# Kernel tuning notes

Measured on AMD Instinct MI355X. Metric: run time of the kernel, lower is better.

The kernel has to match this reference:

```python
import jax, jax.numpy as jnp
import numpy as np

D_MODEL = 1024
D_STATE = 16
D_CONV = 4
EXPAND = 2
D_INNER = EXPAND * D_MODEL
DT_RANK = (D_MODEL + 15) // 16  # ceil(d_model/16) = 64
BATCH = 2
SEQLEN = 1024


def _causal_conv_silu(x, w, b):
    # x: (B, d_inner, L); w: (d_inner, 1, k) depthwise; causal left padding k-1
    k = w.shape[-1]
    y = jax.lax.conv_general_dilated(
        x, w, window_strides=(1,), padding=[(k - 1, 0)],
        dimension_numbers=("NCH", "OIH", "NCH"), feature_group_count=x.shape[1])
    return jax.nn.silu(y + b[None, :, None])


def _ssm_scan(dA, dBx):
    # h_t = dA_t * h_{t-1} + dBx_t, parallel associative scan over L (axis=2)
    def op(e1, e2):
        a1, b1 = e1
        a2, b2 = e2
        return (a1 * a2, a2 * b1 + b2)
    return jax.lax.associative_scan(op, (dA, dBx), axis=2)[1]


def _mamba_dir(xz, conv_w, conv_b, xproj_w, dtproj_w, dt_bias, A_log, Dp):
    d_inner = xz.shape[1] // 2
    x, z = xz[:, :d_inner], xz[:, d_inner:]
    u = _causal_conv_silu(x, conv_w, conv_b)                  # (B, d, L)
    x_dbl = jnp.einsum('bdl,kd->bkl', u, xproj_w)             # (B, dt_rank+2n, L)
    n = A_log.shape[1]
    r = dtproj_w.shape[1]
    delta = jnp.einsum('dr,brl->bdl', dtproj_w, x_dbl[:, :r])
    Bm = x_dbl[:, r:r + n]                                    # (B, n, L)
    Cm = x_dbl[:, r + n:]                                     # (B, n, L)
    delta = jax.nn.softplus(delta + dt_bias[None, :, None])
    A = -jnp.exp(A_log)                                       # (d, n)
    dA = jnp.exp(jnp.einsum('bdl,dn->bdln', delta, A))
    dBx = jnp.einsum('bdl,bnl,bdl->bdln', delta, Bm, u)
    h = _ssm_scan(dA, dBx)                                    # (B, d, L, n)
    y = jnp.einsum('bdln,bnl->bdl', h, Cm)
    y = y + Dp[None, :, None] * u
    return y * jax.nn.silu(z)


def setup_inputs() -> dict:
    key = jax.random.key(0)
    ks = jax.random.split(key, 16)
    s_in = 1.0 / np.sqrt(D_MODEL)
    s_x = 1.0 / np.sqrt(D_INNER)
    dt_std = DT_RANK ** -0.5

    def dt_bias_init(k):
        dt = jnp.exp(jax.random.uniform(k, (D_INNER,)) * (np.log(0.1) - np.log(0.001)) + np.log(0.001))
        dt = jnp.clip(dt, 1e-4, None)
        return dt + jnp.log(-jnp.expm1(-dt))  # inverse softplus

    A_log = jnp.log(jnp.tile(jnp.arange(1, D_STATE + 1, dtype=jnp.float32)[None, :], (D_INNER, 1)))
    inp = {
        'hidden_states': jax.random.normal(ks[0], (BATCH, SEQLEN, D_MODEL), jnp.float32),
        'in_proj_w': jax.random.normal(ks[1], (2 * D_INNER, D_MODEL), jnp.float32) * s_in,
        'conv_w': jax.random.normal(ks[2], (D_INNER, 1, D_CONV), jnp.float32) * 0.3,
        'conv_bias': jnp.zeros((D_INNER,), jnp.float32),
        'x_proj_w': jax.random.normal(ks[3], (DT_RANK + 2 * D_STATE, D_INNER), jnp.float32) * s_x,
        'dt_proj_w': jax.random.uniform(ks[4], (D_INNER, DT_RANK), jnp.float32, -dt_std, dt_std),
        'dt_proj_bias': dt_bias_init(ks[5]),
        'A_log': A_log,
        'D_skip': jnp.ones((D_INNER,), jnp.float32),
        'convb_w': jax.random.normal(ks[6], (D_INNER, 1, D_CONV), jnp.float32) * 0.3,
        'convb_bias': jnp.zeros((D_INNER,), jnp.float32),
        'x_proj_b_w': jax.random.normal(ks[7], (DT_RANK + 2 * D_STATE, D_INNER), jnp.float32) * s_x,
        'dt_proj_b_w': jax.random.uniform(ks[8], (D_INNER, DT_RANK), jnp.float32, -dt_std, dt_std),
        'dt_proj_b_bias': dt_bias_init(ks[9]),
        'A_b_log': A_log,
        'D_b_skip': jnp.ones((D_INNER,), jnp.float32),
        'out_proj_w': jax.random.normal(ks[10], (D_MODEL, D_INNER), jnp.float32) * s_x,
    }
    return inp


def reference(hidden_states, in_proj_w, conv_w, conv_bias, x_proj_w, dt_proj_w,
              dt_proj_bias, A_log, D_skip, convb_w, convb_bias, x_proj_b_w,
              dt_proj_b_w, dt_proj_b_bias, A_b_log, D_b_skip, out_proj_w):
    # in_proj (no bias): (B, 2*d_inner, L)
    xz = jnp.einsum('ed,bld->bel', in_proj_w, hidden_states)
    out_f = _mamba_dir(xz, conv_w, conv_bias, x_proj_w, dt_proj_w, dt_proj_bias, A_log, D_skip)
    out_b = _mamba_dir(xz[:, :, ::-1], convb_w, convb_bias, x_proj_b_w, dt_proj_b_w,
                       dt_proj_b_bias, A_b_log, D_b_skip)[:, :, ::-1]
    # if_divide_out=False: just sum then out_proj (no bias)
    return jnp.einsum('bdl,od->blo', out_f + out_b, out_proj_w)
```

## Files before the change

kernel.cpp:

```cpp
#include <hip/hip_runtime.h>
#include <math.h>


typedef _Float16 f16x8 __attribute__((ext_vector_type(8)));
typedef _Float16 f16x4 __attribute__((ext_vector_type(4)));
typedef float    f32x4 __attribute__((ext_vector_type(4)));

#define SCH 32
#define SCL 32

__device__ __forceinline__ void gload_lds16(const void* g, void* l) {
    __builtin_amdgcn_global_load_lds(
        (const __attribute__((address_space(1))) void*)g,
        (__attribute__((address_space(3))) void*)l, 16, 0, 0);
}

__device__ __forceinline__ float softplus_f(float x) {
    float e = __builtin_amdgcn_exp2f(-fabsf(x) * 1.44269504f);
    return fmaxf(x, 0.f) + __builtin_amdgcn_logf(1.f + e) * 0.69314718f;
}

template<int CTRL>
__device__ __forceinline__ float dpp_add(float x) {
    int s = __builtin_amdgcn_update_dpp(0, __builtin_bit_cast(int, x),
                                        CTRL, 0xF, 0xF, true);
    return x + __builtin_bit_cast(float, s);
}

template<int WMW, int WNW, int FM, int FN>
__global__ __launch_bounds__(256)
void gemm_nt_f16(const _Float16* __restrict__ A, const _Float16* __restrict__ B,
                 float* __restrict__ C, int K, int ldc, long sA, long sC)
{
    constexpr int BM = WMW * FM * 16, BN = WNW * FN * 16;
    constexpr int ACH = BM / 8, NCH = (BM + BN) / 8;
    __shared__ __align__(16) _Float16 lds[(BM + BN) * 64];
    A += (long)blockIdx.z * sA;
    C += (long)blockIdx.z * sC;
    const int m0 = blockIdx.y * BM, n0 = blockIdx.x * BN;
    const int t = threadIdx.x, wid = t >> 6, lane = t & 63;
    const int wm = wid / WNW, wn = wid % WNW;
    const int srow = lane >> 3;
    const int skk  = ((lane & 7) ^ srow) * 8;

    f32x4 acc[FM][FN];
#pragma unroll
    for (int i = 0; i < FM; ++i)
#pragma unroll
        for (int j = 0; j < FN; ++j) acc[i][j] = (f32x4){0.f, 0.f, 0.f, 0.f};

    for (int k0 = 0; k0 < K; k0 += 64) {
#pragma unroll
        for (int c = wid; c < NCH; c += 4) {
            const _Float16* gp = (c < ACH)
                ? A + (long)(m0 + c * 8 + srow) * K + k0 + skk
                : B + (long)(n0 + (c - ACH) * 8 + srow) * K + k0 + skk;
            gload_lds16(gp, lds + c * 512);
        }
        __syncthreads();
#pragma unroll
        for (int kw = 0; kw < 2; ++kw) {
            f16x8 af[FM], bf[FN];
#pragma unroll
            for (int i = 0; i < FM; ++i) {
                int r = wm * FM * 16 + i * 16 + (lane & 15);
                af[i] = *(const f16x8*)(lds + r * 64 +
                        (((kw * 4 + (lane >> 4)) ^ (r & 7)) * 8));
            }
#pragma unroll
            for (int j = 0; j < FN; ++j) {
                int r = wn * FN * 16 + j * 16 + (lane & 15);
                bf[j] = *(const f16x8*)(lds + BM * 64 + r * 64 +
                        (((kw * 4 + (lane >> 4)) ^ (r & 7)) * 8));
            }
#pragma unroll
            for (int i = 0; i < FM; ++i)
#pragma unroll
                for (int j = 0; j < FN; ++j)
                    acc[i][j] = __builtin_amdgcn_mfma_f32_16x16x32_f16(
                        af[i], bf[j], acc[i][j], 0, 0, 0);
        }
        __syncthreads();
    }
#pragma unroll
    for (int i = 0; i < FM; ++i)
#pragma unroll
        for (int j = 0; j < FN; ++j) {
            int n = n0 + wn * FN * 16 + j * 16 + (lane & 15);
            int m = m0 + wm * FM * 16 + i * 16 + (lane >> 4) * 4;
            *(f32x4*)&C[(long)n * ldc + m] = acc[i][j];
        }
}

#define XP_SK 8
__global__ __launch_bounds__(256)
void xproj_f16_kernel(const _Float16* __restrict__ u16, const _Float16* __restrict__ xw16,
                      float* __restrict__ pb)
{
    __shared__ __align__(16) _Float16 Asw[128 * 64];
    __shared__ __align__(16) _Float16 Bsw[96 * 64];
    const int t = threadIdx.x, wid = t >> 6, lane = t & 63;
    const int wm = wid >> 1, wn = wid & 1;
    const int m0 = blockIdx.x * 128;
    const int sk = blockIdx.y, dirb = blockIdx.z;
    const _Float16* ub = u16 + (long)dirb * 2048 * 1024;
    const _Float16* Bw = xw16 + (long)(dirb >> 1) * 96 * 2048;
    const int srow = lane >> 3;
    const int skk  = ((lane & 7) ^ srow) * 8;
    const int lloc = (t & 31) * 4;
    const int kslt = t >> 5;

    f32x4 acc[4][3];
#pragma unroll
    for (int i = 0; i < 4; ++i)
#pragma unroll
        for (int j = 0; j < 3; ++j) acc[i][j] = (f32x4){0.f, 0.f, 0.f, 0.f};

    for (int ks = 0; ks < 2048 / XP_SK; ks += 64) {
        const int k0 = sk * (2048 / XP_SK) + ks;
#pragma unroll
        for (int c = wid; c < 12; c += 4)
            gload_lds16(Bw + (long)(c * 8 + srow) * 2048 + k0 + skk, Bsw + c * 512);
        _Float16 av[8][4];
#pragma unroll
        for (int kk = 0; kk < 8; ++kk) {
            f16x4 v = *(const f16x4*)&ub[(long)(k0 + kslt * 8 + kk) * 1024 + m0 + lloc];
            av[kk][0] = v[0]; av[kk][1] = v[1]; av[kk][2] = v[2]; av[kk][3] = v[3];
        }
#pragma unroll
        for (int q = 0; q < 4; ++q) {
            int l = lloc + q;
            f16x8 h = {av[0][q], av[1][q], av[2][q], av[3][q],
                       av[4][q], av[5][q], av[6][q], av[7][q]};
            *(f16x8*)(Asw + l * 64 + ((kslt ^ (l & 7)) * 8)) = h;
        }
        __syncthreads();
#pragma unroll
        for (int kw = 0; kw < 2; ++kw) {
            f16x8 af[4], bf[3];
#pragma unroll
            for (int i = 0; i < 4; ++i) {
                int r = wm * 64 + i * 16 + (lane & 15);
                af[i] = *(const f16x8*)(Asw + r * 64 +
                        (((kw * 4 + (lane >> 4)) ^ (r & 7)) * 8));
            }
#pragma unroll
            for (int j = 0; j < 3; ++j) {
                int r = wn * 48 + j * 16 + (lane & 15);
                bf[j] = *(const f16x8*)(Bsw + r * 64 +
                        (((kw * 4 + (lane >> 4)) ^ (r & 7)) * 8));
            }
#pragma unroll
            for (int i = 0; i < 4; ++i)
#pragma unroll
                for (int j = 0; j < 3; ++j)
                    acc[i][j] = __builtin_amdgcn_mfma_f32_16x16x32_f16(
                        af[i], bf[j], acc[i][j], 0, 0, 0);
        }
        __syncthreads();
    }
    float* Cp = pb + ((long)sk * 4 + dirb) * 96 * 1024;
#pragma unroll
    for (int i = 0; i < 4; ++i)
#pragma unroll
        for (int j = 0; j < 3; ++j) {
            int n = wn * 48 + j * 16 + (lane & 15);
            int m = m0 + wm * 64 + i * 16 + (lane >> 4) * 4;
            *(f32x4*)&Cp[(long)n * 1024 + m] = acc[i][j];
        }
}

__global__ __launch_bounds__(256)
void xreduce_kernel(const float* __restrict__ pb, float* __restrict__ xdbl)
{
    int f = (blockIdx.x * 256 + threadIdx.x) * 4;
    f32x4 s = (f32x4){0.f, 0.f, 0.f, 0.f};
#pragma unroll
    for (int sk = 0; sk < XP_SK; ++sk)
        s += *(const f32x4*)(pb + (long)sk * 393216 + f);
    *(f32x4*)(xdbl + f) = s;
}

__global__ __launch_bounds__(256)
void dtproj_f16_kernel(const float* __restrict__ xdbl, const _Float16* __restrict__ dw16,
                       const float* __restrict__ bcat, _Float16* __restrict__ delta16)
{
    __shared__ __align__(16) _Float16 Asw[128 * 64];
    __shared__ __align__(16) _Float16 Bsw[128 * 64];
    const int t = threadIdx.x, wid = t >> 6, lane = t & 63;
    const int wm = wid >> 1, wn = wid & 1;
    const int n0 = blockIdx.x * 128, m0 = blockIdx.y * 128;
    const int dirb = blockIdx.z, dir = dirb >> 1;
    const float* Xb = xdbl + (long)dirb * 96 * 1024;
    const _Float16* Bw = dw16 + (long)dir * 2048 * 64;
    const int srow = lane >> 3, skk = ((lane & 7) ^ srow) * 8;
    const int lloc = (t & 31) * 4, kslt = t >> 5;

#pragma unroll
    for (int c = wid; c < 16; c += 4)
        gload_lds16(Bw + (long)(n0 + c * 8 + srow) * 64 + skk, Bsw + c * 512);
    float av[8][4];
#pragma unroll
    for (int kk = 0; kk < 8; ++kk) {
        f32x4 v = *(const f32x4*)&Xb[(long)(kslt * 8 + kk) * 1024 + m0 + lloc];
        av[kk][0] = v.x; av[kk][1] = v.y; av[kk][2] = v.z; av[kk][3] = v.w;
    }
#pragma unroll
    for (int q = 0; q < 4; ++q) {
        int l = lloc + q;
        f16x8 h = {(_Float16)av[0][q], (_Float16)av[1][q], (_Float16)av[2][q],
                   (_Float16)av[3][q], (_Float16)av[4][q], (_Float16)av[5][q],
                   (_Float16)av[6][q], (_Float16)av[7][q]};
        *(f16x8*)(Asw + l * 64 + ((kslt ^ (l & 7)) * 8)) = h;
    }
    __syncthreads();

    f32x4 acc[4][4];
#pragma unroll
    for (int i = 0; i < 4; ++i)
#pragma unroll
        for (int j = 0; j < 4; ++j) acc[i][j] = (f32x4){0.f, 0.f, 0.f, 0.f};
#pragma unroll
    for (int kw = 0; kw < 2; ++kw) {
        f16x8 af[4], bf[4];
#pragma unroll
        for (int i = 0; i < 4; ++i) {
            int r = wm * 64 + i * 16 + (lane & 15);
            af[i] = *(const f16x8*)(Asw + r * 64 +
                    (((kw * 4 + (lane >> 4)) ^ (r & 7)) * 8));
        }
#pragma unroll
        for (int j = 0; j < 4; ++j) {
            int r = wn * 64 + j * 16 + (lane & 15);
            bf[j] = *(const f16x8*)(Bsw + r * 64 +
                    (((kw * 4 + (lane >> 4)) ^ (r & 7)) * 8));
        }
#pragma unroll
        for (int i = 0; i < 4; ++i)
#pragma unroll
            for (int j = 0; j < 4; ++j)
                acc[i][j] = __builtin_amdgcn_mfma_f32_16x16x32_f16(
                    af[i], bf[j], acc[i][j], 0, 0, 0);
    }
    _Float16* Dp = delta16 + (long)dirb * 2048 * 1024;
#pragma unroll
    for (int j = 0; j < 4; ++j) {
        int dd = n0 + wn * 64 + j * 16 + (lane & 15);
        float bm = bcat[dir * 2048 + dd];
#pragma unroll
        for (int i = 0; i < 4; ++i) {
            int m = m0 + wm * 64 + i * 16 + (lane >> 4) * 4;
            f32x4 v = acc[i][j];
            f16x4 o = {(_Float16)softplus_f(v.x + bm), (_Float16)softplus_f(v.y + bm),
                       (_Float16)softplus_f(v.z + bm), (_Float16)softplus_f(v.w + bm)};
            *(f16x4*)&Dp[(long)dd * 1024 + m] = o;
        }
    }
}

__global__ __launch_bounds__(256)
void setup_kernel(const float* __restrict__ hidden, const float* __restrict__ winp,
                  const float* __restrict__ woutp,
                  const float* __restrict__ xwf, const float* __restrict__ xwb,
                  const float* __restrict__ dwf, const float* __restrict__ dwb,
                  const float* __restrict__ bf,  const float* __restrict__ bb,
                  _Float16* __restrict__ H16, _Float16* __restrict__ Win16,
                  _Float16* __restrict__ Wout16,
                  _Float16* __restrict__ xw16, _Float16* __restrict__ dw16,
                  float* __restrict__ bcat)
{
    long i4 = ((long)blockIdx.x * 256 + threadIdx.x) * 4;
    auto cvt4 = [](const float* s) -> f16x4 {
        float4 v = *(const float4*)s;
        return (f16x4){(_Float16)v.x, (_Float16)v.y, (_Float16)v.z, (_Float16)v.w};
    };
    if (i4 < 4194304) *(f16x4*)(Win16 + i4) = cvt4(winp + i4);
    if (i4 < 2097152) {
        *(f16x4*)(H16 + i4)   = cvt4(hidden + i4);
        *(f16x4*)(Wout16 + i4) = cvt4(woutp + i4);
    }
    if (i4 < 196608) {
        *(f16x4*)(xw16 + i4)          = cvt4(xwf + i4);
        *(f16x4*)(xw16 + 196608 + i4) = cvt4(xwb + i4);
    }
    if (i4 < 131072) {
        *(f16x4*)(dw16 + i4)          = cvt4(dwf + i4);
        *(f16x4*)(dw16 + 131072 + i4) = cvt4(dwb + i4);
    }
    if (i4 < 2048) {
        *(float4*)(bcat + i4)        = *(const float4*)(bf + i4);
        *(float4*)(bcat + 2048 + i4) = *(const float4*)(bb + i4);
    }
}

__global__ __launch_bounds__(256)
void conv_silu_kernel(const float* __restrict__ xz,
                      const float* __restrict__ wf, const float* __restrict__ bf,
                      const float* __restrict__ wb, const float* __restrict__ bbk,
                      _Float16* __restrict__ u16)
{
    long idx = (long)blockIdx.x * 256 + threadIdx.x;
    int l = (int)(idx & 1023);
    long r = idx >> 10;
    int d = (int)(r & 2047);
    int b = (int)((r >> 11) & 1);
    int dir = (int)(r >> 12);
    const float* x = xz + ((long)b * 4096 + d) * 1024;
    const float* w = dir ? wb : wf;
    float s = dir ? bbk[d] : bf[d];
    if (dir == 0) {
#pragma unroll
        for (int j = 0; j < 4; ++j) {
            int p = l - 3 + j;
            if (p >= 0) s = fmaf(w[d * 4 + j], x[p], s);
        }
    } else {
#pragma unroll
        for (int j = 0; j < 4; ++j) {
            int src = l - 3 + j;
            if (src >= 0) s = fmaf(w[d * 4 + j], x[1023 - src], s);
        }
    }
    u16[idx] = (_Float16)(s / (1.f + __builtin_amdgcn_exp2f(-s * 1.44269504f)));
}

__global__ __launch_bounds__(256)
void scan_p1_kernel(const _Float16* __restrict__ u16, const _Float16* __restrict__ delta16,
                    const float* __restrict__ xdbl,
                    const float* __restrict__ Alf, const float* __restrict__ Alb,
                    float* __restrict__ hend, float* __restrict__ aprod)
{
    __shared__ _Float16 sD[64][40], sU[64][40];
    __shared__ float sB[32][20];
    const int t = threadIdx.x, wid = t >> 6, lane = t & 63;
    const int nl = lane & 3;
    const int dloc = wid * 16 + (lane >> 2);
    const int dblk = blockIdx.x, chunk = blockIdx.y, dirb = blockIdx.z;
    const int d = dblk * 64 + dloc, dir = dirb >> 1;
    const int T0 = chunk * SCL;
    f32x4 Av = *(const f32x4*)((dir ? Alb : Alf) + d * 16 + nl * 4);
    float An2[4] = {-expf(Av.x) * 1.44269504f, -expf(Av.y) * 1.44269504f,
                    -expf(Av.z) * 1.44269504f, -expf(Av.w) * 1.44269504f};
    const _Float16* dp = delta16 + ((long)dirb * 2048 + dblk * 64) * 1024;
    const _Float16* up = u16    + ((long)dirb * 2048 + dblk * 64) * 1024;
    const float* Bp = xdbl + ((long)dirb * 96 + 64) * 1024;

    {
        int dd = t >> 2, q = t & 3;
        *(f16x8*)&sD[dd][q * 8] = *(const f16x8*)&dp[(long)dd * 1024 + T0 + q * 8];
        *(f16x8*)&sU[dd][q * 8] = *(const f16x8*)&up[(long)dd * 1024 + T0 + q * 8];
    }
#pragma unroll
    for (int rep = 0; rep < 2; ++rep) {
        int ii = rep * 256 + t;
        int n = ii >> 5, tt = ii & 31;
        sB[tt][n] = Bp[(long)n * 1024 + T0 + tt];
    }
    __syncthreads();

    float h[4] = {0.f, 0.f, 0.f, 0.f};
    float S = 0.f;
#pragma unroll 4
    for (int g = 0; g < 8; ++g) {
        f16x4 dlh = *(const f16x4*)&sD[dloc][g * 4];
        f16x4 uuh = *(const f16x4*)&sU[dloc][g * 4];
        float dls[4] = {(float)dlh[0], (float)dlh[1], (float)dlh[2], (float)dlh[3]};
        float uus[4] = {(float)uuh[0], (float)uuh[1], (float)uuh[2], (float)uuh[3]};
#pragma unroll
        for (int r4 = 0; r4 < 4; ++r4) {
            f32x4 Bv = *(const f32x4*)&sB[g * 4 + r4][nl * 4];
            float Bs[4] = {Bv.x, Bv.y, Bv.z, Bv.w};
            float dl = dls[r4], t1 = dl * uus[r4];
            S += dl;
#pragma unroll
            for (int r = 0; r < 4; ++r)
                h[r] = fmaf(__builtin_amdgcn_exp2f(dl * An2[r]), h[r], t1 * Bs[r]);
        }
    }
    long cb = (((long)dirb * SCH + chunk) * 2048 + d) * 16 + nl * 4;
    *(f32x4*)&hend[cb]  = (f32x4){h[0], h[1], h[2], h[3]};
    *(f32x4*)&aprod[cb] = (f32x4){__builtin_amdgcn_exp2f(S * An2[0]),
                                  __builtin_amdgcn_exp2f(S * An2[1]),
                                  __builtin_amdgcn_exp2f(S * An2[2]),
                                  __builtin_amdgcn_exp2f(S * An2[3])};
}

__global__ __launch_bounds__(256)
void scan_carry_kernel(const float* __restrict__ hend, const float* __restrict__ aprod,
                       float* __restrict__ hinit)
{
    int f = blockIdx.x * 256 + threadIdx.x;
    int dn = f & 32767;
    int dirb = f >> 15;
    long src = (long)dirb * SCH * 32768 + dn;
    long dst = (long)(dirb >> 1) * 4194304 + (long)(dirb & 1) * 1048576 + dn;
    float hcur = 0.f;
#pragma unroll
    for (int c = 0; c < SCH; ++c) {
        hinit[dst + (long)c * 32768] = hcur;
        hcur = hend[src + (long)c * 32768]
             + aprod[src + (long)c * 32768] * hcur;
    }
}

__global__ __launch_bounds__(256)
void scan_p3_kernel(const _Float16* __restrict__ u16, const _Float16* __restrict__ delta16,
                    const float* __restrict__ xdbl,
                    const float* __restrict__ Alf, const float* __restrict__ Alb,
                    const float* __restrict__ Df, const float* __restrict__ Db,
                    const float* __restrict__ hinit, _Float16* __restrict__ y16)
{
    __shared__ _Float16 sD[64][40], sU[64][40];
    __shared__ float sB[32][20], sC[32][20];
    const int t = threadIdx.x, wid = t >> 6, lane = t & 63;
    const int nl = lane & 3;
    const int dloc = wid * 16 + (lane >> 2);
    const int dblk = blockIdx.x, chunk = blockIdx.y, dirb = blockIdx.z;
    const int d = dblk * 64 + dloc, dir = dirb >> 1;
    const int T0 = chunk * SCL;
    f32x4 Av = *(const f32x4*)((dir ? Alb : Alf) + d * 16 + nl * 4);
    float An2[4] = {-expf(Av.x) * 1.44269504f, -expf(Av.y) * 1.44269504f,
                    -expf(Av.z) * 1.44269504f, -expf(Av.w) * 1.44269504f};
    const float Dd = (dir ? Db : Df)[d];
    const _Float16* dp = delta16 + ((long)dirb * 2048 + dblk * 64) * 1024;
    const _Float16* up = u16    + ((long)dirb * 2048 + dblk * 64) * 1024;
    const float* Bp = xdbl + ((long)dirb * 96 + 64) * 1024;
    const float* Cp = xdbl + ((long)dirb * 96 + 80) * 1024;
    _Float16* yrow = y16 + ((long)dirb * 2048 + d) * 1024;

    {
        int dd = t >> 2, q = t & 3;
        *(f16x8*)&sD[dd][q * 8] = *(const f16x8*)&dp[(long)dd * 1024 + T0 + q * 8];
        *(f16x8*)&sU[dd][q * 8] = *(const f16x8*)&up[(long)dd * 1024 + T0 + q * 8];
    }
#pragma unroll
    for (int rep = 0; rep < 2; ++rep) {
        int ii = rep * 256 + t;
        int n = ii >> 5, tt = ii & 31;
        sB[tt][n] = Bp[(long)n * 1024 + T0 + tt];
        sC[tt][n] = Cp[(long)n * 1024 + T0 + tt];
    }
    long cb = (long)(dirb >> 1) * 4194304 + (long)(dirb & 1) * 1048576
            + (long)chunk * 32768 + (long)d * 16 + nl * 4;
    f32x4 h0v = *(const f32x4*)&hinit[cb];
    float h[4] = {h0v.x, h0v.y, h0v.z, h0v.w};
    const bool m[4] = {nl == 0, nl == 1, nl == 2, nl == 3};
    __syncthreads();

#pragma unroll 4
    for (int g = 0; g < 8; ++g) {
        f16x4 dlh = *(const f16x4*)&sD[dloc][g * 4];
        f16x4 uuh = *(const f16x4*)&sU[dloc][g * 4];
        float dls[4] = {(float)dlh[0], (float)dlh[1], (float)dlh[2], (float)dlh[3]};
        float uus[4] = {(float)uuh[0], (float)uuh[1], (float)uuh[2], (float)uuh[3]};
        float keep = 0.f;
#pragma unroll
        for (int r4 = 0; r4 < 4; ++r4) {
            f32x4 Bv = *(const f32x4*)&sB[g * 4 + r4][nl * 4];
            f32x4 Cv = *(const f32x4*)&sC[g * 4 + r4][nl * 4];
            float Bs[4] = {Bv.x, Bv.y, Bv.z, Bv.w};
            float Cs[4] = {Cv.x, Cv.y, Cv.z, Cv.w};
            float dl = dls[r4], uu = uus[r4];
            float t1 = dl * uu;
#pragma unroll
            for (int r = 0; r < 4; ++r)
                h[r] = fmaf(__builtin_amdgcn_exp2f(dl * An2[r]), h[r], t1 * Bs[r]);
            float p = h[0] * Cs[0];
            p = fmaf(h[1], Cs[1], p);
            p = fmaf(h[2], Cs[2], p);
            p = fmaf(h[3], Cs[3], p);
            p = dpp_add<0xB1>(p);
            p = dpp_add<0x4E>(p);
            float fy = fmaf(Dd, uu, p);
            keep = m[r4] ? fy : keep;
        }
        yrow[T0 + g * 4 + nl] = (_Float16)keep;
    }
}

__global__ __launch_bounds__(256)
void combine_T_kernel(const float* __restrict__ xz, const _Float16* __restrict__ y16,
                      _Float16* __restrict__ GT)
{
    __shared__ float Ls[64][65];
    const int d0 = blockIdx.x * 64, l0 = blockIdx.y * 64, b = blockIdx.z;
    const int t = threadIdx.x;
#pragma unroll
    for (int rep = 0; rep < 4; ++rep) {
        int i = rep * 256 + t;
        int dl = i >> 4;
        int lq = (i & 15) * 4;
        const float* zp = xz + ((long)b * 4096 + 2048 + d0 + dl) * 1024 + l0 + lq;
        const _Float16* yfp = y16 + ((long)(b)     * 2048 + d0 + dl) * 1024 + l0 + lq;
        const _Float16* ybp = y16 + ((long)(2 + b) * 2048 + d0 + dl) * 1024 + (1020 - l0 - lq);
        float4 vz = *(const float4*)zp;
        f16x4 vf = *(const f16x4*)yfp;
        f16x4 vb = *(const f16x4*)ybp;
        float zz[4]  = {vz.x, vz.y, vz.z, vz.w};
        float ff[4]  = {(float)vf[0], (float)vf[1], (float)vf[2], (float)vf[3]};
        float bbv[4] = {(float)vb[3], (float)vb[2], (float)vb[1], (float)vb[0]};
#pragma unroll
        for (int qq = 0; qq < 4; ++qq) {
            float z = zz[qq];
            float sz = z / (1.f + __builtin_amdgcn_exp2f(-z * 1.44269504f));
            Ls[dl][lq + qq] = sz * (ff[qq] + bbv[qq]);
        }
    }
    __syncthreads();
#pragma unroll
    for (int rep = 0; rep < 4; ++rep) {
        int i = rep * 256 + t;
        int ll = i >> 4;
        int dq = (i & 15) * 4;
        f16x4 h = {(_Float16)Ls[dq][ll], (_Float16)Ls[dq + 1][ll],
                   (_Float16)Ls[dq + 2][ll], (_Float16)Ls[dq + 3][ll]};
        *(f16x4*)(GT + ((long)(b * 1024 + l0 + ll)) * 2048 + d0 + dq) = h;
    }
}

extern "C" void kernel_launch(void* const* d_in, const int* in_sizes, int n_in,
                              void* d_out, int out_size, void* d_ws, size_t ws_size,
                              hipStream_t stream)
{
    const float* hidden   = (const float*)d_in[0];
    const float* inproj_w = (const float*)d_in[1];
    const float* conv_w   = (const float*)d_in[2];
    const float* conv_b   = (const float*)d_in[3];
    const float* xproj_w  = (const float*)d_in[4];
    const float* dtproj_w = (const float*)d_in[5];
    const float* dt_bias  = (const float*)d_in[6];
    const float* A_log    = (const float*)d_in[7];
    const float* D_skip   = (const float*)d_in[8];
    const float* convb_w  = (const float*)d_in[9];
    const float* convb_b  = (const float*)d_in[10];
    const float* xprojb_w = (const float*)d_in[11];
    const float* dtprojb_w= (const float*)d_in[12];
    const float* dtb_bias = (const float*)d_in[13];
    const float* Ab_log   = (const float*)d_in[14];
    const float* Db_skip  = (const float*)d_in[15];
    const float* outproj_w= (const float*)d_in[16];
    float* out = (float*)d_out;

    float* ws    = (float*)d_ws;
    float* xz    = ws;
    float* u     = ws + 8388608;
    float* xdbl  = ws + 16777216;
    float* delta = ws + 17170432;
    float* y     = ws + 25559040;
    _Float16* H16    = (_Float16*)u;
    _Float16* Win16  = (_Float16*)(u + 1048576);
    _Float16* u16    = (_Float16*)(u + 3145728);
    _Float16* Wout16 = (_Float16*)(u + 7340032);
    _Float16* delta16 = (_Float16*)delta;
    float*    xpb     = delta + 4194304;
    _Float16* GT      = (_Float16*)delta;
    _Float16* dw16  = (_Float16*)y;
    float*    bcat  = y + 131072;
    _Float16* xw16  = (_Float16*)(y + 135168);
    float* hend  = y;
    float* aprod = y + 4194304;
    _Float16* y16 = (_Float16*)y;
    float* hinit = xz;

    hipLaunchKernelGGL(setup_kernel, dim3(4096), dim3(256), 0, stream,
        hidden, inproj_w, outproj_w, xproj_w, xprojb_w, dtproj_w, dtprojb_w,
        dt_bias, dtb_bias, H16, Win16, Wout16, xw16, dw16, bcat);

    hipLaunchKernelGGL((gemm_nt_f16<2, 2, 4, 4>),
        dim3(32, 8, 2), dim3(256), 0, stream,
        H16, Win16, xz, 1024, 1024, 1048576L, 4194304L);

    hipLaunchKernelGGL(conv_silu_kernel, dim3(32768), dim3(256), 0, stream,
        xz, conv_w, conv_b, convb_w, convb_b, u16);

    hipLaunchKernelGGL(xproj_f16_kernel, dim3(8, XP_SK, 4), dim3(256), 0, stream,
        u16, xw16, xpb);
    hipLaunchKernelGGL(xreduce_kernel, dim3(384), dim3(256), 0, stream,
        xpb, xdbl);

    hipLaunchKernelGGL(dtproj_f16_kernel, dim3(16, 8, 4), dim3(256), 0, stream,
        xdbl, dw16, bcat, delta16);

    hipLaunchKernelGGL(scan_p1_kernel, dim3(32, SCH, 4), dim3(256), 0, stream,
        u16, delta16, xdbl, A_log, Ab_log, hend, aprod);
    hipLaunchKernelGGL(scan_carry_kernel, dim3(512), dim3(256), 0, stream,
        hend, aprod, hinit);
    hipLaunchKernelGGL(scan_p3_kernel, dim3(32, SCH, 4), dim3(256), 0, stream,
        u16, delta16, xdbl, A_log, Ab_log, D_skip, Db_skip, hinit, y16);

    hipLaunchKernelGGL(combine_T_kernel, dim3(32, 16, 2), dim3(256), 0, stream,
        xz, y16, GT);

    hipLaunchKernelGGL((gemm_nt_f16<4, 1, 2, 4>),
        dim3(32, 8, 1), dim3(256), 0, stream,
        Wout16, GT, out, 2048, 1024, 0L, 0L);
}
```

Before: 180.8 us.

## Store in_proj output and scan chunk carries in fp16 to cut traffic

```diff
diff --git a/kernel.cpp b/kernel.cpp
--- a/kernel.cpp
+++ b/kernel.cpp
@@ -27,10 +27,10 @@
     return x + __builtin_bit_cast(float, s);
 }
 
-template<int WMW, int WNW, int FM, int FN>
+template<int WMW, int WNW, int FM, int FN, typename CT>
 __global__ __launch_bounds__(256)
 void gemm_nt_f16(const _Float16* __restrict__ A, const _Float16* __restrict__ B,
-                 float* __restrict__ C, int K, int ldc, long sA, long sC)
+                 CT* __restrict__ C, int K, int ldc, long sA, long sC)
 {
     constexpr int BM = WMW * FM * 16, BN = WNW * FN * 16;
     constexpr int ACH = BM / 8, NCH = (BM + BN) / 8;
@@ -88,7 +88,13 @@
         for (int j = 0; j < FN; ++j) {
             int n = n0 + wn * FN * 16 + j * 16 + (lane & 15);
             int m = m0 + wm * FM * 16 + i * 16 + (lane >> 4) * 4;
-            *(f32x4*)&C[(long)n * ldc + m] = acc[i][j];
+            f32x4 v = acc[i][j];
+            if constexpr (__is_same(CT, float)) {
+                *(f32x4*)&C[(long)n * ldc + m] = v;
+            } else {
+                f16x4 h = {(_Float16)v.x, (_Float16)v.y, (_Float16)v.z, (_Float16)v.w};
+                *(f16x4*)&C[(long)n * ldc + m] = h;
+            }
         }
 }
 
@@ -294,7 +300,7 @@
 }
 
 __global__ __launch_bounds__(256)
-void conv_silu_kernel(const float* __restrict__ xz,
+void conv_silu_kernel(const _Float16* __restrict__ xz16,
                       const float* __restrict__ wf, const float* __restrict__ bf,
                       const float* __restrict__ wb, const float* __restrict__ bbk,
                       _Float16* __restrict__ u16)
@@ -305,20 +311,20 @@
     int d = (int)(r & 2047);
     int b = (int)((r >> 11) & 1);
     int dir = (int)(r >> 12);
-    const float* x = xz + ((long)b * 4096 + d) * 1024;
+    const _Float16* x = xz16 + ((long)b * 4096 + d) * 1024;
     const float* w = dir ? wb : wf;
     float s = dir ? bbk[d] : bf[d];
     if (dir == 0) {
 #pragma unroll
         for (int j = 0; j < 4; ++j) {
             int p = l - 3 + j;
-            if (p >= 0) s = fmaf(w[d * 4 + j], x[p], s);
+            if (p >= 0) s = fmaf(w[d * 4 + j], (float)x[p], s);
         }
     } else {
 #pragma unroll
         for (int j = 0; j < 4; ++j) {
             int src = l - 3 + j;
-            if (src >= 0) s = fmaf(w[d * 4 + j], x[1023 - src], s);
+            if (src >= 0) s = fmaf(w[d * 4 + j], (float)x[1023 - src], s);
         }
     }
     u16[idx] = (_Float16)(s / (1.f + __builtin_amdgcn_exp2f(-s * 1.44269504f)));
@@ -328,7 +334,7 @@
 void scan_p1_kernel(const _Float16* __restrict__ u16, const _Float16* __restrict__ delta16,
                     const float* __restrict__ xdbl,
                     const float* __restrict__ Alf, const float* __restrict__ Alb,
-                    float* __restrict__ hend, float* __restrict__ aprod)
+                    _Float16* __restrict__ hend16, _Float16* __restrict__ aprod16)
 {
     __shared__ _Float16 sD[64][40], sU[64][40];
     __shared__ float sB[32][20];
@@ -378,28 +384,30 @@
         }
     }
     long cb = (((long)dirb * SCH + chunk) * 2048 + d) * 16 + nl * 4;
-    *(f32x4*)&hend[cb]  = (f32x4){h[0], h[1], h[2], h[3]};
-    *(f32x4*)&aprod[cb] = (f32x4){__builtin_amdgcn_exp2f(S * An2[0]),
-                                  __builtin_amdgcn_exp2f(S * An2[1]),
-                                  __builtin_amdgcn_exp2f(S * An2[2]),
-                                  __builtin_amdgcn_exp2f(S * An2[3])};
-}
-
-__global__ __launch_bounds__(256)
-void scan_carry_kernel(const float* __restrict__ hend, const float* __restrict__ aprod,
-                       float* __restrict__ hinit)
+    f16x4 he = {(_Float16)h[0], (_Float16)h[1], (_Float16)h[2], (_Float16)h[3]};
+    f16x4 ap = {(_Float16)__builtin_amdgcn_exp2f(S * An2[0]),
+                (_Float16)__builtin_amdgcn_exp2f(S * An2[1]),
+                (_Float16)__builtin_amdgcn_exp2f(S * An2[2]),
+                (_Float16)__builtin_amdgcn_exp2f(S * An2[3])};
+    *(f16x4*)&hend16[cb]  = he;
+    *(f16x4*)&aprod16[cb] = ap;
+}
+
+__global__ __launch_bounds__(256)
+void scan_carry_kernel(const _Float16* __restrict__ hend16,
+                       const _Float16* __restrict__ aprod16,
+                       _Float16* __restrict__ hinit16)
 {
     int f = blockIdx.x * 256 + threadIdx.x;
     int dn = f & 32767;
     int dirb = f >> 15;
-    long src = (long)dirb * SCH * 32768 + dn;
-    long dst = (long)(dirb >> 1) * 4194304 + (long)(dirb & 1) * 1048576 + dn;
+    long base = (long)dirb * SCH * 32768 + dn;
     float hcur = 0.f;
 #pragma unroll
     for (int c = 0; c < SCH; ++c) {
-        hinit[dst + (long)c * 32768] = hcur;
-        hcur = hend[src + (long)c * 32768]
-             + aprod[src + (long)c * 32768] * hcur;
+        hinit16[base + (long)c * 32768] = (_Float16)hcur;
+        hcur = (float)hend16[base + (long)c * 32768]
+             + (float)aprod16[base + (long)c * 32768] * hcur;
     }
 }
 
@@ -408,7 +416,7 @@
                     const float* __restrict__ xdbl,
                     const float* __restrict__ Alf, const float* __restrict__ Alb,
                     const float* __restrict__ Df, const float* __restrict__ Db,
-                    const float* __restrict__ hinit, _Float16* __restrict__ y16)
+                    const _Float16* __restrict__ hinit16, _Float16* __restrict__ y16)
 {
     __shared__ _Float16 sD[64][40], sU[64][40];
     __shared__ float sB[32][20], sC[32][20];
@@ -440,10 +448,9 @@
         sB[tt][n] = Bp[(long)n * 1024 + T0 + tt];
         sC[tt][n] = Cp[(long)n * 1024 + T0 + tt];
     }
-    long cb = (long)(dirb >> 1) * 4194304 + (long)(dirb & 1) * 1048576
-            + (long)chunk * 32768 + (long)d * 16 + nl * 4;
-    f32x4 h0v = *(const f32x4*)&hinit[cb];
-    float h[4] = {h0v.x, h0v.y, h0v.z, h0v.w};
+    long cb = (((long)dirb * SCH + chunk) * 2048 + d) * 16 + nl * 4;
+    f16x4 h0v = *(const f16x4*)&hinit16[cb];
+    float h[4] = {(float)h0v[0], (float)h0v[1], (float)h0v[2], (float)h0v[3]};
     const bool m[4] = {nl == 0, nl == 1, nl == 2, nl == 3};
     __syncthreads();
 
@@ -479,7 +486,7 @@
 }
 
 __global__ __launch_bounds__(256)
-void combine_T_kernel(const float* __restrict__ xz, const _Float16* __restrict__ y16,
+void combine_T_kernel(const _Float16* __restrict__ xz16, const _Float16* __restrict__ y16,
                       _Float16* __restrict__ GT)
 {
     __shared__ float Ls[64][65];
@@ -490,13 +497,13 @@
         int i = rep * 256 + t;
         int dl = i >> 4;
         int lq = (i & 15) * 4;
-        const float* zp = xz + ((long)b * 4096 + 2048 + d0 + dl) * 1024 + l0 + lq;
+        const _Float16* zp  = xz16 + ((long)b * 4096 + 2048 + d0 + dl) * 1024 + l0 + lq;
         const _Float16* yfp = y16 + ((long)(b)     * 2048 + d0 + dl) * 1024 + l0 + lq;
         const _Float16* ybp = y16 + ((long)(2 + b) * 2048 + d0 + dl) * 1024 + (1020 - l0 - lq);
-        float4 vz = *(const float4*)zp;
+        f16x4 vz = *(const f16x4*)zp;
         f16x4 vf = *(const f16x4*)yfp;
         f16x4 vb = *(const f16x4*)ybp;
-        float zz[4]  = {vz.x, vz.y, vz.z, vz.w};
+        float zz[4]  = {(float)vz[0], (float)vz[1], (float)vz[2], (float)vz[3]};
         float ff[4]  = {(float)vf[0], (float)vf[1], (float)vf[2], (float)vf[3]};
         float bbv[4] = {(float)vb[3], (float)vb[2], (float)vb[1], (float)vb[0]};
 #pragma unroll
@@ -547,31 +554,32 @@
     float* xdbl  = ws + 16777216;
     float* delta = ws + 17170432;
     float* y     = ws + 25559040;
-    _Float16* H16    = (_Float16*)u;
-    _Float16* Win16  = (_Float16*)(u + 1048576);
-    _Float16* u16    = (_Float16*)(u + 3145728);
-    _Float16* Wout16 = (_Float16*)(u + 7340032);
+    _Float16* xz16 = (_Float16*)xz;
+    _Float16* H16     = (_Float16*)u;
+    _Float16* Win16   = (_Float16*)(u + 1048576);
+    _Float16* u16     = (_Float16*)(u + 3145728);
+    _Float16* Wout16  = (_Float16*)(u + 7340032);
+    _Float16* hinit16 = (_Float16*)u;
     _Float16* delta16 = (_Float16*)delta;
     float*    xpb     = delta + 4194304;
     _Float16* GT      = (_Float16*)delta;
     _Float16* dw16  = (_Float16*)y;
     float*    bcat  = y + 131072;
     _Float16* xw16  = (_Float16*)(y + 135168);
-    float* hend  = y;
-    float* aprod = y + 4194304;
-    _Float16* y16 = (_Float16*)y;
-    float* hinit = xz;
+    _Float16* hend16  = (_Float16*)y;
+    _Float16* aprod16 = (_Float16*)(y + 2097152);
+    _Float16* y16     = (_Float16*)y;
 
     hipLaunchKernelGGL(setup_kernel, dim3(4096), dim3(256), 0, stream,
         hidden, inproj_w, outproj_w, xproj_w, xprojb_w, dtproj_w, dtprojb_w,
         dt_bias, dtb_bias, H16, Win16, Wout16, xw16, dw16, bcat);
 
-    hipLaunchKernelGGL((gemm_nt_f16<2, 2, 4, 4>),
+    hipLaunchKernelGGL((gemm_nt_f16<2, 2, 4, 4, _Float16>),
         dim3(32, 8, 2), dim3(256), 0, stream,
-        H16, Win16, xz, 1024, 1024, 1048576L, 4194304L);
+        H16, Win16, xz16, 1024, 1024, 1048576L, 4194304L);
 
     hipLaunchKernelGGL(conv_silu_kernel, dim3(32768), dim3(256), 0, stream,
-        xz, conv_w, conv_b, convb_w, convb_b, u16);
+        xz16, conv_w, conv_b, convb_w, convb_b, u16);
 
     hipLaunchKernelGGL(xproj_f16_kernel, dim3(8, XP_SK, 4), dim3(256), 0, stream,
         u16, xw16, xpb);
@@ -582,16 +590,16 @@
         xdbl, dw16, bcat, delta16);
 
     hipLaunchKernelGGL(scan_p1_kernel, dim3(32, SCH, 4), dim3(256), 0, stream,
-        u16, delta16, xdbl, A_log, Ab_log, hend, aprod);
+        u16, delta16, xdbl, A_log, Ab_log, hend16, aprod16);
     hipLaunchKernelGGL(scan_carry_kernel, dim3(512), dim3(256), 0, stream,
-        hend, aprod, hinit);
+        hend16, aprod16, hinit16);
     hipLaunchKernelGGL(scan_p3_kernel, dim3(32, SCH, 4), dim3(256), 0, stream,
-        u16, delta16, xdbl, A_log, Ab_log, D_skip, Db_skip, hinit, y16);
+        u16, delta16, xdbl, A_log, Ab_log, D_skip, Db_skip, hinit16, y16);
 
     hipLaunchKernelGGL(combine_T_kernel, dim3(32, 16, 2), dim3(256), 0, stream,
-        xz, y16, GT);
-
-    hipLaunchKernelGGL((gemm_nt_f16<4, 1, 2, 4>),
+        xz16, y16, GT);
+
+    hipLaunchKernelGGL((gemm_nt_f16<4, 1, 2, 4, float>),
         dim3(32, 8, 1), dim3(256), 0, stream,
         Wout16, GT, out, 2048, 1024, 0L, 0L);
 }
```

Result: faster. 175.7 us (-2.8%).
